# Performance work log

Measured on AMD Instinct MI355X. Metric: run time of the kernel, lower is better.

Reference implementation:

```python
import jax, jax.numpy as jnp
import numpy as np

N = 50000      # nodes
E = 640000     # edges
F_IN = 128     # in_channels
H = 128        # hidden / layer size
G = 64         # graphs in batch
OUT = 5        # classes


def _lin_init(key, fan_in, fan_out):
    s = 1.0 / np.sqrt(fan_in)
    kw, kb = jax.random.split(key)
    w = jax.random.uniform(kw, (fan_in, fan_out), jnp.float32, -s, s)
    b = jax.random.uniform(kb, (fan_out,), jnp.float32, -s, s)
    return w, b


def setup_inputs() -> dict:
    key = jax.random.key(0)
    ks = jax.random.split(key, 8)
    x = jax.random.normal(ks[0], (N, F_IN), jnp.float32)
    edge_index = jax.random.randint(ks[1], (2, E), 0, N, dtype=jnp.int64)
    # sorted graph assignment, every graph nonempty (sorted_randint-style)
    batch = (jnp.arange(N, dtype=jnp.int64) * G) // N
    c0w1, c0b1 = _lin_init(ks[2], F_IN, H)
    c0w2, c0b2 = _lin_init(ks[3], H, H)
    c1w1, c1b1 = _lin_init(ks[4], H, H)
    c1w2, c1b2 = _lin_init(ks[5], H, H)
    lw, lb = _lin_init(ks[6], H, OUT)
    return {"x": x, "edge_index": edge_index, "batch": batch,
            "conv0_w1": c0w1, "conv0_b1": c0b1, "conv0_w2": c0w2, "conv0_b2": c0b2,
            "conv1_w1": c1w1, "conv1_b1": c1b1, "conv1_w2": c1w2, "conv1_b2": c1b2,
            "lin_w": lw, "lin_b": lb}


def reference(x, edge_index, batch,
              conv0_w1, conv0_b1, conv0_w2, conv0_b2,
              conv1_w1, conv1_b1, conv1_w2, conv1_b2,
              lin_w, lin_b):
    src, dst = edge_index[0], edge_index[1]

    def gin_conv(h, w1, b1, w2, b2):
        # scatter-add neighbor aggregation: out_i = sum_{(j->i) in E} h_j
        agg = jax.ops.segment_sum(h[src], dst, num_segments=N)
        z = agg + h  # GIN with eps = 0 (train_eps=False)
        # PyG MLP (2 layers, eval mode): Linear -> ReLU -> Linear
        z = jax.nn.relu(z @ w1 + b1) @ w2 + b2
        return jax.nn.relu(z)  # outer .relu() in forward

    h = gin_conv(x, conv0_w1, conv0_b1, conv0_w2, conv0_b2)
    h = gin_conv(h, conv1_w1, conv1_b1, conv1_w2, conv1_b2)
    # global max pool over each graph (all segments nonempty by construction)
    pooled = jax.ops.segment_max(h, batch, num_segments=G)
    # dropout p=0.3 is a no-op in eval mode
    return pooled @ lin_w + lin_b
```

## Files before the change

### kernel.cpp

```cpp
#include <hip/hip_runtime.h>
#include <hip/hip_bf16.h>

#define N_NODES 50000
#define N_EDGES 640000
#define HDIM 128
#define NGRAPH 64
#define NOUT 5
#define CAP 64

typedef __attribute__((ext_vector_type(4))) short short4v;
typedef __attribute__((ext_vector_type(8))) short short8v;
typedef __attribute__((ext_vector_type(4))) float float4v;

__device__ inline float blo(unsigned u) { return __uint_as_float(u << 16); }
__device__ inline float bhi(unsigned u) { return __uint_as_float(u & 0xffff0000u); }
__device__ inline unsigned short f2b(float f) {
    __hip_bfloat16 h = __float2bfloat16(f);
    return *reinterpret_cast<unsigned short*>(&h);
}

__device__ inline int xcd_swz(int bid, int n) {
    int x = bid & 7, d = bid >> 3;
    int q = n >> 3, rem = n & 7;
    return (x < rem) ? x * (q + 1) + d : rem * (q + 1) + (x - rem) * q + d;
}


__global__ void k_scatter_b(const int* __restrict__ src, const int* __restrict__ dst,
                            int* __restrict__ cur, int* __restrict__ adj) {
    int e = blockIdx.x * blockDim.x + threadIdx.x;
    if (e < N_EDGES) {
        int d = dst[e];
        int pos = atomicAdd(&cur[d], 1);
        adj[(size_t)d * CAP + pos] = src[e];
    }
}

__global__ __launch_bounds__(256) void k_prep(const float* __restrict__ x,
                                              const float* __restrict__ w0a,
                                              const float* __restrict__ w0b,
                                              const float* __restrict__ w1a,
                                              const float* __restrict__ w1b,
                                              int* __restrict__ zero_p, int nz,
                                              unsigned short* __restrict__ wf,
                                              unsigned short* __restrict__ xb) {
    int i = xcd_swz(blockIdx.x, gridDim.x) * 256 + threadIdx.x;
    if (i < nz) zero_p[i] = 0;
    if (i < 4 * 2048) {
        int m = i >> 11, rem = i & 2047;
        int c = rem >> 8, ks = (rem >> 6) & 3, lane = rem & 63;
        int r = lane & 15, g = lane >> 4;
        int n = c * 16 + r, k0 = ks * 32 + 4 * g;
        const float* w = (m == 0) ? w0a : (m == 1) ? w0b : (m == 2) ? w1a : w1b;
        unsigned short v[8];
#pragma unroll
        for (int j = 0; j < 4; j++) {
            v[j]     = f2b(w[(k0 + j) * HDIM + n]);
            v[4 + j] = f2b(w[(k0 + 16 + j) * HDIM + n]);
        }
        uint4 o;
        o.x = v[0] | ((unsigned)v[1] << 16);
        o.y = v[2] | ((unsigned)v[3] << 16);
        o.z = v[4] | ((unsigned)v[5] << 16);
        o.w = v[6] | ((unsigned)v[7] << 16);
        ((uint4*)wf)[i] = o;
    }
    if (i < N_NODES * 16) {
        int row = i >> 4;
        int p0 = (i & 15) * 8;
        int ks = p0 >> 5, g2 = (p0 >> 3) & 3;
        const float* xr = x + (size_t)row * HDIM + ks * 32 + 4 * g2;
        float4 a = *(const float4*)xr;
        float4 b = *(const float4*)(xr + 16);
        uint4 o;
        o.x = f2b(a.x) | ((unsigned)f2b(a.y) << 16);
        o.y = f2b(a.z) | ((unsigned)f2b(a.w) << 16);
        o.z = f2b(b.x) | ((unsigned)f2b(b.y) << 16);
        o.w = f2b(b.z) | ((unsigned)f2b(b.w) << 16);
        *(uint4*)&xb[(size_t)row * HDIM + p0] = o;
    }
}

__global__ __launch_bounds__(256) void k_agg_b(const unsigned short* __restrict__ h,
                                               const int* __restrict__ cnt,
                                               const int* __restrict__ adj,
                                               unsigned short* __restrict__ out) {
    int node = xcd_swz(blockIdx.x, gridDim.x) * 16 + (threadIdx.x >> 4);
    if (node >= N_NODES) return;
    int c = (threadIdx.x & 15) * 8;
    const unsigned short* hc = h + c;
    uint4 sv = *(const uint4*)(hc + (size_t)node * HDIM);
    float acc[8];
    acc[0] = blo(sv.x); acc[1] = bhi(sv.x);
    acc[2] = blo(sv.y); acc[3] = bhi(sv.y);
    acc[4] = blo(sv.z); acc[5] = bhi(sv.z);
    acc[6] = blo(sv.w); acc[7] = bhi(sv.w);
#define ACC8(v) do { \
        acc[0] += blo(v.x); acc[1] += bhi(v.x); \
        acc[2] += blo(v.y); acc[3] += bhi(v.y); \
        acc[4] += blo(v.z); acc[5] += bhi(v.z); \
        acc[6] += blo(v.w); acc[7] += bhi(v.w); } while (0)
    int s = node * CAP;
    int e = s + cnt[node];
    int k = s;
    for (; k + 4 <= e; k += 4) {
        int j0 = adj[k], j1 = adj[k + 1], j2 = adj[k + 2], j3 = adj[k + 3];
        uint4 v0 = *(const uint4*)(hc + (size_t)j0 * HDIM);
        uint4 v1 = *(const uint4*)(hc + (size_t)j1 * HDIM);
        uint4 v2 = *(const uint4*)(hc + (size_t)j2 * HDIM);
        uint4 v3 = *(const uint4*)(hc + (size_t)j3 * HDIM);
        ACC8(v0); ACC8(v1); ACC8(v2); ACC8(v3);
    }
    for (; k < e; k++) {
        int j = adj[k];
        uint4 v = *(const uint4*)(hc + (size_t)j * HDIM);
        ACC8(v);
    }
#undef ACC8
    uint4 o;
    o.x = f2b(acc[0]) | ((unsigned)f2b(acc[1]) << 16);
    o.y = f2b(acc[2]) | ((unsigned)f2b(acc[3]) << 16);
    o.z = f2b(acc[4]) | ((unsigned)f2b(acc[5]) << 16);
    o.w = f2b(acc[6]) | ((unsigned)f2b(acc[7]) << 16);
    *(uint4*)&out[(size_t)node * HDIM + c] = o;
}

template <bool POOL>
__global__ __launch_bounds__(256, 4) void k_mlp(const unsigned short* __restrict__ A,
                                                const unsigned short* __restrict__ w1f,
                                                const unsigned short* __restrict__ w2f,
                                                const float* __restrict__ b1,
                                                const float* __restrict__ b2,
                                                unsigned short* __restrict__ C,
                                                unsigned* __restrict__ pooled) {
    __shared__ uint4 lw[2048];
    int tid = threadIdx.x;
    int lane = tid & 63;
    int w = tid >> 6;
    int r = lane & 15;
    int g = lane >> 4;
    int Lb = xcd_swz(blockIdx.x, gridDim.x);
    int base = Lb * 64 + w * 16;
    int row = base + r;
    int rowc = (row < N_NODES) ? row : (N_NODES - 1);

    short8v fbv[4];
    {
        const unsigned short* arow = A + (size_t)rowc * HDIM;
#pragma unroll
        for (int ks = 0; ks < 4; ks++)
            fbv[ks] = *(const short8v*)(arow + ks * 32 + g * 8);
    }

    {
        const uint4* g1 = (const uint4*)w1f;
#pragma unroll
        for (int i = 0; i < 8; i++) lw[tid + i * 256] = g1[tid + i * 256];
    }
    __syncthreads();

    float4v acc1[8];
#pragma unroll
    for (int c = 0; c < 8; c++) acc1[c] = (float4v){0.f, 0.f, 0.f, 0.f};
#pragma unroll
    for (int ks = 0; ks < 4; ks++)
#pragma unroll
        for (int c = 0; c < 8; c++) {
            short8v fa = *(const short8v*)&lw[(c * 4 + ks) * 64 + lane];
            acc1[c] = __builtin_amdgcn_mfma_f32_16x16x32_bf16(fa, fbv[ks], acc1[c], 0, 0, 0);
        }

    short8v fb2[4];
#pragma unroll
    for (int ks = 0; ks < 4; ks++) {
        float4 bA = *(const float4*)&b1[(2 * ks) * 16 + 4 * g];
        float4 bB = *(const float4*)&b1[(2 * ks + 1) * 16 + 4 * g];
        short8v f;
        f[0] = (short)f2b(fmaxf(acc1[2 * ks][0] + bA.x, 0.f));
        f[1] = (short)f2b(fmaxf(acc1[2 * ks][1] + bA.y, 0.f));
        f[2] = (short)f2b(fmaxf(acc1[2 * ks][2] + bA.z, 0.f));
        f[3] = (short)f2b(fmaxf(acc1[2 * ks][3] + bA.w, 0.f));
        f[4] = (short)f2b(fmaxf(acc1[2 * ks + 1][0] + bB.x, 0.f));
        f[5] = (short)f2b(fmaxf(acc1[2 * ks + 1][1] + bB.y, 0.f));
        f[6] = (short)f2b(fmaxf(acc1[2 * ks + 1][2] + bB.z, 0.f));
        f[7] = (short)f2b(fmaxf(acc1[2 * ks + 1][3] + bB.w, 0.f));
        fb2[ks] = f;
    }
    __syncthreads();

    {
        const uint4* g2 = (const uint4*)w2f;
#pragma unroll
        for (int i = 0; i < 8; i++) lw[tid + i * 256] = g2[tid + i * 256];
    }
    __syncthreads();

    float4v acc2[8];
#pragma unroll
    for (int c = 0; c < 8; c++) acc2[c] = (float4v){0.f, 0.f, 0.f, 0.f};
#pragma unroll
    for (int ks = 0; ks < 4; ks++)
#pragma unroll
        for (int c = 0; c < 8; c++) {
            short8v fa = *(const short8v*)&lw[(c * 4 + ks) * 64 + lane];
            acc2[c] = __builtin_amdgcn_mfma_f32_16x16x32_bf16(fa, fb2[ks], acc2[c], 0, 0, 0);
        }

    if constexpr (!POOL) {
        bool ok = (row < N_NODES);
#pragma unroll
        for (int ks = 0; ks < 4; ks++) {
            float4 bA = *(const float4*)&b2[ks * 32 + 4 * g];
            float4 bB = *(const float4*)&b2[ks * 32 + 16 + 4 * g];
            uint4 st;
            st.x = f2b(fmaxf(acc2[2 * ks][0] + bA.x, 0.f)) |
                   ((unsigned)f2b(fmaxf(acc2[2 * ks][1] + bA.y, 0.f)) << 16);
            st.y = f2b(fmaxf(acc2[2 * ks][2] + bA.z, 0.f)) |
                   ((unsigned)f2b(fmaxf(acc2[2 * ks][3] + bA.w, 0.f)) << 16);
            st.z = f2b(fmaxf(acc2[2 * ks + 1][0] + bB.x, 0.f)) |
                   ((unsigned)f2b(fmaxf(acc2[2 * ks + 1][1] + bB.y, 0.f)) << 16);
            st.w = f2b(fmaxf(acc2[2 * ks + 1][2] + bB.z, 0.f)) |
                   ((unsigned)f2b(fmaxf(acc2[2 * ks + 1][3] + bB.w, 0.f)) << 16);
            if (ok) *(uint4*)&C[(size_t)row * HDIM + ks * 32 + g * 8] = st;
        }
    } else {
        unsigned gid0 = ((unsigned)base * 64u) / 50000u;
        unsigned gid1 = ((unsigned)(base + 15) * 64u) / 50000u;
        bool fast = (base + 15 < N_NODES) && (gid0 == gid1);
        if (fast) {
            float vm[8][4];
#pragma unroll
            for (int c = 0; c < 8; c++) {
                int ks = c >> 1, h2 = c & 1;
                float4 bv = *(const float4*)&b2[ks * 32 + h2 * 16 + 4 * g];
                float bb[4] = {bv.x, bv.y, bv.z, bv.w};
#pragma unroll
                for (int i = 0; i < 4; i++)
                    vm[c][i] = fmaxf(acc2[c][i] + bb[i], 0.f);
            }
#pragma unroll
            for (int mask = 1; mask <= 8; mask <<= 1)
#pragma unroll
                for (int c = 0; c < 8; c++)
#pragma unroll
                    for (int i = 0; i < 4; i++)
                        vm[c][i] = fmaxf(vm[c][i], __shfl_xor(vm[c][i], mask));
            if (r == 0) {
                unsigned* pool = pooled + gid0 * HDIM;
#pragma unroll
                for (int c = 0; c < 8; c++) {
                    int p = (c >> 1) * 32 + g * 8 + (c & 1) * 4;
#pragma unroll
                    for (int i = 0; i < 4; i++)
                        atomicMax(&pool[p + i], __float_as_uint(vm[c][i]));
                }
            }
        } else if (row < N_NODES) {
            unsigned gid = ((unsigned)row * 64u) / 50000u;
            unsigned* pool = pooled + gid * HDIM;
#pragma unroll
            for (int c = 0; c < 8; c++) {
                int ks = c >> 1, h2 = c & 1;
                float4 bv = *(const float4*)&b2[ks * 32 + h2 * 16 + 4 * g];
                float bb[4] = {bv.x, bv.y, bv.z, bv.w};
                int p = ks * 32 + g * 8 + h2 * 4;
#pragma unroll
                for (int i = 0; i < 4; i++)
                    atomicMax(&pool[p + i],
                              __float_as_uint(fmaxf(acc2[c][i] + bb[i], 0.f)));
            }
        }
    }
}

__global__ void k_final(const float* __restrict__ pooled, const float* __restrict__ lw,
                        const float* __restrict__ lb, float* __restrict__ out) {
    int t = threadIdx.x;
    if (t >= NGRAPH * NOUT) return;
    int g = t / NOUT, o = t % NOUT;
    float acc = lb[o];
    for (int p = 0; p < HDIM; p++) {
        int col = (p & 0x60) | ((p & 4) << 2) | ((p & 0x18) >> 1) | (p & 3);
        acc = fmaf(pooled[g * HDIM + p], lw[col * NOUT + o], acc);
    }
    out[t] = acc;
}

extern "C" void kernel_launch(void* const* d_in, const int* in_sizes, int n_in,
                              void* d_out, int out_size, void* d_ws, size_t ws_size,
                              hipStream_t stream) {
    const float* x    = (const float*)d_in[0];
    const int*   ei   = (const int*)d_in[1];
    const int*   srcv = ei;
    const int*   dstv = ei + N_EDGES;
    const float* c0w1 = (const float*)d_in[3];
    const float* c0b1 = (const float*)d_in[4];
    const float* c0w2 = (const float*)d_in[5];
    const float* c0b2 = (const float*)d_in[6];
    const float* c1w1 = (const float*)d_in[7];
    const float* c1b1 = (const float*)d_in[8];
    const float* c1w2 = (const float*)d_in[9];
    const float* c1b2 = (const float*)d_in[10];
    const float* lw   = (const float*)d_in[11];
    const float* lb   = (const float*)d_in[12];
    float* out = (float*)d_out;

    char* ws = (char*)d_ws;
    int* cur      = (int*)(ws);
    float* pooled = (float*)(cur + N_NODES);
    int* adj      = (int*)(ws + 1ull * 1024 * 1024);
    unsigned short* wf = (unsigned short*)(ws + 14ull * 1024 * 1024);
    unsigned short* xb = (unsigned short*)(ws + 17ull * 1024 * 1024);
    unsigned short* b0 = (unsigned short*)(ws + 30ull * 1024 * 1024);
    unsigned short* b1 = (unsigned short*)(ws + 43ull * 1024 * 1024);

    const int NZ  = N_NODES + NGRAPH * HDIM;
    const int NBE = (N_EDGES + 255) / 256;
    const int NBL = (N_NODES + 63) / 64;
    const int NBA = (N_NODES + 15) / 16;
    const int NBC = (N_NODES * 16 + 255) / 256;

    k_prep<<<NBC, 256, 0, stream>>>(x, c0w1, c0w2, c1w1, c1w2, cur, NZ, wf, xb);

    k_scatter_b<<<NBE, 256, 0, stream>>>(srcv, dstv, cur, adj);

    k_agg_b<<<NBA, 256, 0, stream>>>(xb, cur, adj, b0);
    k_mlp<false><<<NBL, 256, 0, stream>>>(b0, wf, wf + 16384, c0b1, c0b2, b1, nullptr);

    k_agg_b<<<NBA, 256, 0, stream>>>(b1, cur, adj, b0);
    k_mlp<true><<<NBL, 256, 0, stream>>>(b0, wf + 32768, wf + 49152, c1b1, c1b2,
                                         nullptr, (unsigned*)pooled);

    k_final<<<1, 320, 0, stream>>>(pooled, lw, lb, out);
}
```

Measured before the change: 240.0 us.

## Fuse edge scatter into prep kernel and read MLP weights directly from global

```diff
diff --git a/kernel.cpp b/kernel.cpp
--- a/kernel.cpp
+++ b/kernel.cpp
@@ -26,14 +26,9 @@
 }
 
 
-__global__ void k_scatter_b(const int* __restrict__ src, const int* __restrict__ dst,
-                            int* __restrict__ cur, int* __restrict__ adj) {
-    int e = blockIdx.x * blockDim.x + threadIdx.x;
-    if (e < N_EDGES) {
-        int d = dst[e];
-        int pos = atomicAdd(&cur[d], 1);
-        adj[(size_t)d * CAP + pos] = src[e];
-    }
+__global__ void k_zero(int* __restrict__ p, int n) {
+    int i = blockIdx.x * 256 + threadIdx.x;
+    if (i < n) p[i] = 0;
 }
 
 __global__ __launch_bounds__(256) void k_prep(const float* __restrict__ x,
@@ -41,11 +36,18 @@
                                               const float* __restrict__ w0b,
                                               const float* __restrict__ w1a,
                                               const float* __restrict__ w1b,
-                                              int* __restrict__ zero_p, int nz,
+                                              const int* __restrict__ srcv,
+                                              const int* __restrict__ dstv,
+                                              int* __restrict__ cur,
+                                              int* __restrict__ adj,
                                               unsigned short* __restrict__ wf,
                                               unsigned short* __restrict__ xb) {
-    int i = xcd_swz(blockIdx.x, gridDim.x) * 256 + threadIdx.x;
-    if (i < nz) zero_p[i] = 0;
+    int i = blockIdx.x * 256 + threadIdx.x;
+    if (i < N_EDGES) {
+        int d = dstv[i];
+        int pos = atomicAdd(&cur[d], 1);
+        adj[(size_t)d * CAP + pos] = srcv[i];
+    }
     if (i < 4 * 2048) {
         int m = i >> 11, rem = i & 2047;
         int c = rem >> 8, ks = (rem >> 6) & 3, lane = rem & 63;
@@ -133,7 +135,6 @@
                                                 const float* __restrict__ b2,
                                                 unsigned short* __restrict__ C,
                                                 unsigned* __restrict__ pooled) {
-    __shared__ uint4 lw[2048];
     int tid = threadIdx.x;
     int lane = tid & 63;
     int w = tid >> 6;
@@ -144,6 +145,9 @@
     int row = base + r;
     int rowc = (row < N_NODES) ? row : (N_NODES - 1);
 
+    const short8v* W1 = (const short8v*)w1f;
+    const short8v* W2 = (const short8v*)w2f;
+
     short8v fbv[4];
     {
         const unsigned short* arow = A + (size_t)rowc * HDIM;
@@ -152,23 +156,15 @@
             fbv[ks] = *(const short8v*)(arow + ks * 32 + g * 8);
     }
 
-    {
-        const uint4* g1 = (const uint4*)w1f;
-#pragma unroll
-        for (int i = 0; i < 8; i++) lw[tid + i * 256] = g1[tid + i * 256];
-    }
-    __syncthreads();
-
     float4v acc1[8];
 #pragma unroll
     for (int c = 0; c < 8; c++) acc1[c] = (float4v){0.f, 0.f, 0.f, 0.f};
 #pragma unroll
     for (int ks = 0; ks < 4; ks++)
 #pragma unroll
-        for (int c = 0; c < 8; c++) {
-            short8v fa = *(const short8v*)&lw[(c * 4 + ks) * 64 + lane];
-            acc1[c] = __builtin_amdgcn_mfma_f32_16x16x32_bf16(fa, fbv[ks], acc1[c], 0, 0, 0);
-        }
+        for (int c = 0; c < 8; c++)
+            acc1[c] = __builtin_amdgcn_mfma_f32_16x16x32_bf16(
+                W1[(c * 4 + ks) * 64 + lane], fbv[ks], acc1[c], 0, 0, 0);
 
     short8v fb2[4];
 #pragma unroll
@@ -186,14 +182,6 @@
         f[7] = (short)f2b(fmaxf(acc1[2 * ks + 1][3] + bB.w, 0.f));
         fb2[ks] = f;
     }
-    __syncthreads();
-
-    {
-        const uint4* g2 = (const uint4*)w2f;
-#pragma unroll
-        for (int i = 0; i < 8; i++) lw[tid + i * 256] = g2[tid + i * 256];
-    }
-    __syncthreads();
 
     float4v acc2[8];
 #pragma unroll
@@ -201,10 +189,9 @@
 #pragma unroll
     for (int ks = 0; ks < 4; ks++)
 #pragma unroll
-        for (int c = 0; c < 8; c++) {
-            short8v fa = *(const short8v*)&lw[(c * 4 + ks) * 64 + lane];
-            acc2[c] = __builtin_amdgcn_mfma_f32_16x16x32_bf16(fa, fb2[ks], acc2[c], 0, 0, 0);
-        }
+        for (int c = 0; c < 8; c++)
+            acc2[c] = __builtin_amdgcn_mfma_f32_16x16x32_bf16(
+                W2[(c * 4 + ks) * 64 + lane], fb2[ks], acc2[c], 0, 0, 0);
 
     if constexpr (!POOL) {
         bool ok = (row < N_NODES);
@@ -315,14 +302,15 @@
     unsigned short* b1 = (unsigned short*)(ws + 43ull * 1024 * 1024);
 
     const int NZ  = N_NODES + NGRAPH * HDIM;
-    const int NBE = (N_EDGES + 255) / 256;
+    const int NBZ = (NZ + 255) / 256;
     const int NBL = (N_NODES + 63) / 64;
     const int NBA = (N_NODES + 15) / 16;
     const int NBC = (N_NODES * 16 + 255) / 256;
 
-    k_prep<<<NBC, 256, 0, stream>>>(x, c0w1, c0w2, c1w1, c1w2, cur, NZ, wf, xb);
-
-    k_scatter_b<<<NBE, 256, 0, stream>>>(srcv, dstv, cur, adj);
+    k_zero<<<NBZ, 256, 0, stream>>>(cur, NZ);
+
+    k_prep<<<NBC, 256, 0, stream>>>(x, c0w1, c0w2, c1w1, c1w2,
+                                    srcv, dstv, cur, adj, wf, xb);
 
     k_agg_b<<<NBA, 256, 0, stream>>>(xb, cur, adj, b0);
     k_mlp<false><<<NBL, 256, 0, stream>>>(b0, wf, wf + 16384, c0b1, c0b2, b1, nullptr);
```

Result: no change. 244.6 us (+1.9%).
